# Kernel optimization log

Hardware: AMD Instinct MI355X
Metric: run time of the kernel (lower is better)

Reference implementation:

```python
import jax, jax.numpy as jnp
import numpy as np

GRID = 24          # grid_size = sqrt(N-1)
N = GRID * GRID + 1
C = 768
H = 12
D = C // H
WINDOW = 7
B = 32


def build_local_mask(seq_len, grid_size, window_size):
    # patch (row, col) coordinates for tokens 1..N-1
    idx = np.arange(seq_len - 1)
    row = idx // grid_size
    col = idx % grid_size
    r = window_size // 2
    # local window: |dr| <= r and |dc| <= r (matches the torch double loop)
    patch_mask = (np.abs(row[:, None] - row[None, :]) <= r) & \
                 (np.abs(col[:, None] - col[None, :]) <= r)
    mask = np.zeros((seq_len, seq_len), dtype=bool)
    mask[1:, 1:] = patch_mask
    mask[0, :] = True   # CLS attends to all
    mask[:, 0] = True   # all attend to CLS
    return jnp.asarray(mask)


def setup_inputs() -> dict:
    key = jax.random.key(0)
    kx, kqkv, kproj = jax.random.split(key, 3)
    x = jax.random.normal(kx, (B, N, C), dtype=jnp.float32)
    W_qkv = jax.random.normal(kqkv, (C, 3 * C), dtype=jnp.float32) * 0.02
    W_proj = jax.random.normal(kproj, (C, C), dtype=jnp.float32) * 0.02
    b_proj = jnp.zeros((C,), dtype=jnp.float32)
    mask = build_local_mask(N, GRID, WINDOW)
    return {"x": x, "W_qkv": W_qkv, "W_proj": W_proj, "b_proj": b_proj, "mask": mask}


def reference(x, W_qkv, W_proj, b_proj, mask):
    Bb, Nn, Cc = x.shape
    scale = 1.0 / jnp.sqrt(jnp.asarray(D, dtype=x.dtype))
    qkv = (x @ W_qkv).reshape(Bb, Nn, 3, H, D)
    qkv = jnp.transpose(qkv, (2, 0, 3, 1, 4))  # [3, B, H, N, D]
    q, k, v = qkv[0], qkv[1], qkv[2]
    attn = jnp.einsum('bhnd,bhmd->bhnm', q, k) * scale
    attn = jnp.where(mask[None, None, :, :], attn, jnp.asarray(-jnp.inf, dtype=attn.dtype))
    attn = jax.nn.softmax(attn, axis=-1)
    out = jnp.einsum('bhnm,bhmd->bhnd', attn, v)  # [B, H, N, D]
    out = jnp.transpose(out, (0, 2, 1, 3)).reshape(Bb, Nn, Cc)
    return out @ W_proj + b_proj
```

## Files before the change

kernel.cpp:

```cpp
#include <hip/hip_runtime.h>
#include <stdint.h>

#define GRID_S 24
#define NTOK   577
#define CDIM   768
#define HEADS  12
#define DHEAD  64
#define BATCH  32

#define MREAL  (BATCH*NTOK)
#define MTILES 145
#define MPAD   (MTILES*128)
#define KDIM   768
#define NQKV   2304
#define VTP    584

typedef __attribute__((ext_vector_type(4))) float         f32x4;
typedef __attribute__((ext_vector_type(8))) short         s16x8;
typedef __attribute__((ext_vector_type(4))) unsigned int  u32x4;
typedef __attribute__((address_space(1))) const void g_void;
typedef __attribute__((address_space(3))) void lds_void;

__device__ __forceinline__ unsigned short f2bf(float f) {
    unsigned int u = __float_as_uint(f);
    u += 0x7fffu + ((u >> 16) & 1u);
    return (unsigned short)(u >> 16);
}
__device__ __forceinline__ float bf2f(unsigned short h) {
    return __uint_as_float(((unsigned int)h) << 16);
}

extern "C" __global__ void __launch_bounds__(256)
k_cast_x(const float* __restrict__ x, unsigned short* __restrict__ xb) {
    const long long n4 = (long long)MPAD * CDIM / 4;
    const long long v4 = (long long)MREAL * CDIM / 4;
    long long i = (long long)blockIdx.x * blockDim.x + threadIdx.x;
    const long long stride = (long long)gridDim.x * blockDim.x;
    for (; i < n4; i += stride) {
        float4 v = (i < v4) ? ((const float4*)x)[i] : make_float4(0.f, 0.f, 0.f, 0.f);
        ushort4 o;
        o.x = f2bf(v.x); o.y = f2bf(v.y); o.z = f2bf(v.z); o.w = f2bf(v.w);
        ((ushort4*)xb)[i] = o;
    }
}

extern "C" __global__ void __launch_bounds__(256)
k_tcast(const float* __restrict__ W, unsigned short* __restrict__ WT, int ncol, int n) {
    int i = blockIdx.x * blockDim.x + threadIdx.x;
    const int stride = gridDim.x * blockDim.x;
    for (; i < n; i += stride) {
        const int c = i / KDIM;
        const int k = i - c * KDIM;
        WT[i] = f2bf(W[(long long)k * ncol + c]);
    }
}

__device__ __forceinline__ void gemm_core(const unsigned short* __restrict__ A,
                                          const unsigned short* __restrict__ BT,
                                          int m0, int n0,
                                          unsigned short* As, unsigned short* Bs,
                                          f32x4 acc[4][4]) {
    const int tid  = threadIdx.x;
    const int lane = tid & 63;
    const int wid  = tid >> 6;
    const int wm = wid >> 1, wn = wid & 1;
    const int lrow = lane & 15;
    const int kh   = (lane >> 4) * 8;
    const int srow = (lane >> 2);
    const int scol = (lane & 3) * 16;

#pragma unroll
    for (int i = 0; i < 4; i++)
#pragma unroll
        for (int j = 0; j < 4; j++)
            acc[i][j] = (f32x4){0.f, 0.f, 0.f, 0.f};

    for (int k0 = 0; k0 < KDIM; k0 += 32) {
#pragma unroll
        for (int c = 0; c < 2; ++c) {
            const int chunk = wid * 2 + c;
            const int row   = chunk * 16 + srow;
            const char* ga = (const char*)(A  + (long long)(m0 + row) * KDIM + k0) + scol;
            const char* gb = (const char*)(BT + (long long)(n0 + row) * KDIM + k0) + scol;
            __builtin_amdgcn_global_load_lds((g_void*)ga, (lds_void*)((char*)As + chunk * 1024), 16, 0, 0);
            __builtin_amdgcn_global_load_lds((g_void*)gb, (lds_void*)((char*)Bs + chunk * 1024), 16, 0, 0);
        }
        __syncthreads();

        s16x8 af[4], bq[4];
#pragma unroll
        for (int f = 0; f < 4; ++f) {
            af[f] = *(const s16x8*)(As + (wm * 64 + f * 16 + lrow) * 32 + kh);
            bq[f] = *(const s16x8*)(Bs + (wn * 64 + f * 16 + lrow) * 32 + kh);
        }
#pragma unroll
        for (int i = 0; i < 4; i++)
#pragma unroll
            for (int j = 0; j < 4; j++)
                acc[i][j] = __builtin_amdgcn_mfma_f32_16x16x32_bf16(af[i], bq[j], acc[i][j], 0, 0, 0);
        __syncthreads();
    }
}

extern "C" __global__ void __launch_bounds__(256)
k_gemm_qkv(const unsigned short* __restrict__ A, const unsigned short* __restrict__ BT,
           unsigned short* __restrict__ Qb, unsigned short* __restrict__ Kb,
           unsigned short* __restrict__ Vb) {
    __shared__ unsigned short As[128 * 32];
    __shared__ unsigned short Bs[128 * 32];
    const int m0 = blockIdx.x * 128;
    const int n0 = blockIdx.y * 128;
    f32x4 acc[4][4];
    gemm_core(A, BT, m0, n0, As, Bs, acc);

    const int lane = threadIdx.x & 63;
    const int wid  = threadIdx.x >> 6;
    const int wm = wid >> 1, wn = wid & 1;
    const int lrow = lane & 15;
#pragma unroll
    for (int fi = 0; fi < 4; ++fi) {
        const int mbase = m0 + wm * 64 + fi * 16 + (lane >> 4) * 4;
#pragma unroll
        for (int fj = 0; fj < 4; ++fj) {
            const int cb  = n0 + wn * 64 + fj * 16;
            const int s   = cb / 768;
            const int rem = cb - s * 768;
            const int h   = rem >> 6;
            const int d   = (rem & 63) + lrow;
            const float sc = (s == 0) ? 0.125f : 1.0f;
            unsigned short* dst = (s == 0) ? Qb : (s == 1) ? Kb : Vb;
#pragma unroll
            for (int i = 0; i < 4; i++) {
                const int m = mbase + i;
                if (m < MREAL) {
                    const int b  = m / NTOK;
                    const int nn = m - b * NTOK;
                    dst[(((long long)(b * HEADS + h)) * NTOK + nn) * DHEAD + d] = f2bf(acc[fi][fj][i] * sc);
                }
            }
        }
    }
}

extern "C" __global__ void __launch_bounds__(256)
k_gemm_proj(const unsigned short* __restrict__ A, const unsigned short* __restrict__ BT,
            const float* __restrict__ bias, float* __restrict__ out) {
    __shared__ unsigned short As[128 * 32];
    __shared__ unsigned short Bs[128 * 32];
    const int m0 = blockIdx.x * 128;
    const int n0 = blockIdx.y * 128;
    f32x4 acc[4][4];
    gemm_core(A, BT, m0, n0, As, Bs, acc);

    const int lane = threadIdx.x & 63;
    const int wid  = threadIdx.x >> 6;
    const int wm = wid >> 1, wn = wid & 1;
    const int lrow = lane & 15;
#pragma unroll
    for (int fi = 0; fi < 4; ++fi) {
        const int mbase = m0 + wm * 64 + fi * 16 + (lane >> 4) * 4;
#pragma unroll
        for (int fj = 0; fj < 4; ++fj) {
            const int col = n0 + wn * 64 + fj * 16 + lrow;
            const float bv = bias[col];
#pragma unroll
            for (int i = 0; i < 4; i++) {
                const int m = mbase + i;
                if (m < MREAL) out[(long long)m * CDIM + col] = acc[fi][fj][i] + bv;
            }
        }
    }
}

extern "C" __global__ void __launch_bounds__(256)
k_vtrans(const unsigned short* __restrict__ Vb, unsigned short* __restrict__ Vt) {
    const int NB = 145;
    const int total = 384 * 64 * NB;
    int idx = blockIdx.x * 256 + threadIdx.x;
    if (idx >= total) return;
    const int bh = idx / (64 * NB);
    const int r  = idx - bh * 64 * NB;
    const int d  = r / NB;
    const int nb = r - d * NB;
    const int n0 = nb * 4 + 1;
    const unsigned short* src = Vb + ((long long)bh * NTOK) * 64 + d;
    ushort4 o;
    o.x = src[(long long)min(n0 + 0, NTOK - 1) * 64];
    o.y = src[(long long)min(n0 + 1, NTOK - 1) * 64];
    o.z = src[(long long)min(n0 + 2, NTOK - 1) * 64];
    o.w = src[(long long)min(n0 + 3, NTOK - 1) * 64];
    *(ushort4*)(Vt + ((long long)bh * 64 + d) * VTP + (n0 - 1)) = o;
}

extern "C" __global__ void __launch_bounds__(256)
k_attn2(const unsigned short* __restrict__ Qb, const unsigned short* __restrict__ Kb,
        const unsigned short* __restrict__ Vb, const unsigned short* __restrict__ Vt,
        unsigned short* __restrict__ AO) {
    const int l   = threadIdx.x & 63;
    const int w   = threadIdx.x >> 6;
    const int bh  = blockIdx.x;
    const int qt  = blockIdx.y;
    const int qbase = qt * 64 + w * 16;
    if (qbase >= NTOK) return;
    const int q15 = l & 15;
    const int hi  = l >> 4;
    const int kh  = hi * 8;

    const unsigned short* Qh  = Qb + (long long)bh * NTOK * 64;
    const unsigned short* Kh  = Kb + (long long)bh * NTOK * 64;
    const unsigned short* Vbh = Vb + (long long)bh * NTOK * 64;
    const unsigned short* Vh  = Vt + (long long)bh * 64 * VTP;

    const int qn_frag = min(qbase + q15, NTOK - 1);
    const s16x8 qf0 = *(const s16x8*)(Qh + (long long)qn_frag * 64 + kh);
    const s16x8 qf1 = *(const s16x8*)(Qh + (long long)qn_frag * 64 + 32 + kh);

    const int q_n = qbase + q15;
    const bool q_is_cls = (q_n == 0);
    int pr = 0, pc = 0;
    {
        const int p = (q_n >= 1 ? min(q_n, NTOK - 1) : 1) - 1;
        pr = p / GRID_S; pc = p - pr * GRID_S;
    }

    int ks, ke;
    if (qbase == 0) { ks = 1; ke = NTOK; }
    else {
        const int nlo = qbase, nhi = min(qbase + 15, NTOK - 1);
        const int prmin = (nlo - 1) / GRID_S, prmax = (nhi - 1) / GRID_S;
        const int rlo = max(0, prmin - 3), rhi = min(GRID_S - 1, prmax + 3);
        ks = 1 + rlo * GRID_S; ke = 1 + (rhi + 1) * GRID_S;
    }

    float s0 = 0.f;
    {
        const s16x8 k0a = *(const s16x8*)(Kh + kh);
        const s16x8 k0b = *(const s16x8*)(Kh + 32 + kh);
#pragma unroll
        for (int j = 0; j < 8; ++j) {
            s0 += bf2f((unsigned short)qf0[j]) * bf2f((unsigned short)k0a[j]);
            s0 += bf2f((unsigned short)qf1[j]) * bf2f((unsigned short)k0b[j]);
        }
    }
    s0 += __shfl_xor(s0, 16, 64);
    s0 += __shfl_xor(s0, 32, 64);
    const float e0 = __expf(s0);

    float e0q[4];
#pragma unroll
    for (int i = 0; i < 4; ++i) e0q[i] = __shfl(e0, (hi << 2) + i, 64);

    f32x4 Oacc[4];
#pragma unroll
    for (int dt = 0; dt < 4; ++dt) {
        const float v0 = bf2f(Vbh[dt * 16 + q15]);
        f32x4 t; t[0] = e0q[0]*v0; t[1] = e0q[1]*v0; t[2] = e0q[2]*v0; t[3] = e0q[3]*v0;
        Oacc[dt] = t;
    }

    float dsum = 0.f;
    const int nch = (ke - ks + 31) >> 5;
    for (int ch = 0; ch < nch; ++ch) {
        const int cb = ks + (ch << 5);
        f32x4 ct0 = (f32x4){0,0,0,0}, ct1 = (f32x4){0,0,0,0};

#define QK_TILE(TB, CT) {                                                          \
            const int key = min((TB) + q15, NTOK - 1);                             \
            const unsigned short* kp_ = Kh + (long long)key * 64 + kh;             \
            const s16x8 ka  = *(const s16x8*)kp_;                                  \
            const s16x8 kb2 = *(const s16x8*)(kp_ + 32);                           \
            f32x4 c = __builtin_amdgcn_mfma_f32_16x16x32_bf16(ka,  qf0, (f32x4){0,0,0,0}, 0,0,0); \
            c = __builtin_amdgcn_mfma_f32_16x16x32_bf16(kb2, qf1, c, 0,0,0);       \
            _Pragma("unroll")                                                      \
            for (int i = 0; i < 4; ++i) {                                          \
                const int kk  = (TB) + (hi << 2) + i;                              \
                const int kpp = kk - 1;                                            \
                const int kr  = kpp / GRID_S;                                      \
                const int kc  = kpp - kr * GRID_S;                                 \
                const bool win = ((unsigned)(kr - pr + 3) <= 6u) && ((unsigned)(kc - pc + 3) <= 6u); \
                const bool valid = (kk < ke) && (q_is_cls || win);                 \
                const float e = valid ? __expf(c[i]) : 0.f;                        \
                CT[i] = e; dsum += e;                                              \
            } }

        QK_TILE(cb, ct0)
        if (cb + 16 < ke) QK_TILE(cb + 16, ct1)
#undef QK_TILE

        float pv[8];
#pragma unroll
        for (int j = 0; j < 8; ++j) {
            const int src = ((((hi & 1) << 3) + j) >> 2) * 16 + q15;
            const float a0 = __shfl(ct0[j & 3], src, 64);
            const float a1 = __shfl(ct1[j & 3], src, 64);
            pv[j] = (hi & 2) ? a1 : a0;
        }
        u32x4 paw;
#pragma unroll
        for (int t = 0; t < 4; ++t)
            paw[t] = (unsigned)f2bf(pv[2 * t]) | ((unsigned)f2bf(pv[2 * t + 1]) << 16);
        const s16x8 pa16 = __builtin_bit_cast(s16x8, paw);

        const int gvb = cb - 1 + kh;
#pragma unroll
        for (int dt = 0; dt < 4; ++dt) {
            const s16x8 vf = *(const s16x8*)(Vh + (long long)(dt * 16 + q15) * VTP + gvb);
            Oacc[dt] = __builtin_amdgcn_mfma_f32_16x16x32_bf16(pa16, vf, Oacc[dt], 0, 0, 0);
        }
    }

    dsum += __shfl_xor(dsum, 16, 64);
    dsum += __shfl_xor(dsum, 32, 64);
    const float tot = e0 + dsum;
    float rq[4];
#pragma unroll
    for (int i = 0; i < 4; ++i) rq[i] = 1.f / __shfl(tot, (hi << 2) + i, 64);

    const int b = bh / HEADS, h = bh - b * HEADS;
#pragma unroll
    for (int i = 0; i < 4; ++i) {
        const int n = qbase + (hi << 2) + i;
        if (n < NTOK) {
#pragma unroll
            for (int dt = 0; dt < 4; ++dt)
                AO[((long long)(b * NTOK + n)) * CDIM + h * 64 + dt * 16 + q15] =
                    f2bf(Oacc[dt][i] * rq[i]);
        }
    }
}

extern "C" void kernel_launch(void* const* d_in, const int* in_sizes, int n_in,
                              void* d_out, int out_size, void* d_ws, size_t ws_size,
                              hipStream_t stream) {
    (void)in_sizes; (void)n_in; (void)out_size; (void)ws_size;
    const float* x     = (const float*)d_in[0];
    const float* Wqkv  = (const float*)d_in[1];
    const float* Wproj = (const float*)d_in[2];
    const float* bproj = (const float*)d_in[3];
    float* out = (float*)d_out;
    char*  ws  = (char*)d_ws;

    unsigned short* xb  = (unsigned short*)(ws);
    unsigned short* wqT = (unsigned short*)(ws + 28508160LL);
    unsigned short* wpT = (unsigned short*)(ws + 32047104LL);
    unsigned short* Qb  = (unsigned short*)(ws + 33226752LL);
    unsigned short* Kb  = (unsigned short*)(ws + 61593600LL);
    unsigned short* Vb  = (unsigned short*)(ws + 89960448LL);
    unsigned short* AO  = (unsigned short*)(ws + 118327296LL);
    unsigned short* Vt  = (unsigned short*)(ws);

    hipLaunchKernelGGL(k_cast_x,  dim3(2048), dim3(256), 0, stream, x, xb);
    hipLaunchKernelGGL(k_tcast,   dim3(2048), dim3(256), 0, stream, Wqkv, wqT, NQKV, KDIM * NQKV);
    hipLaunchKernelGGL(k_tcast,   dim3(1024), dim3(256), 0, stream, Wproj, wpT, CDIM, KDIM * CDIM);
    hipLaunchKernelGGL(k_gemm_qkv, dim3(MTILES, NQKV / 128), dim3(256), 0, stream, xb, wqT, Qb, Kb, Vb);
    hipLaunchKernelGGL(k_vtrans,  dim3((384 * 64 * 145 + 255) / 256), dim3(256), 0, stream, Vb, Vt);
    hipLaunchKernelGGL(k_attn2,   dim3(384, 10), dim3(256), 0, stream, Qb, Kb, Vb, Vt, AO);
    hipLaunchKernelGGL(k_gemm_proj, dim3(MTILES, CDIM / 128), dim3(256), 0, stream, AO, wpT, bproj, out);
}
```

Before: 417.6 us.

## Double-buffer GEMM LDS tiles and transpose V through an LDS tile

```diff
diff --git a/kernel.cpp b/kernel.cpp
--- a/kernel.cpp
+++ b/kernel.cpp
@@ -75,23 +75,30 @@
         for (int j = 0; j < 4; j++)
             acc[i][j] = (f32x4){0.f, 0.f, 0.f, 0.f};
 
-    for (int k0 = 0; k0 < KDIM; k0 += 32) {
-#pragma unroll
-        for (int c = 0; c < 2; ++c) {
-            const int chunk = wid * 2 + c;
-            const int row   = chunk * 16 + srow;
-            const char* ga = (const char*)(A  + (long long)(m0 + row) * KDIM + k0) + scol;
-            const char* gb = (const char*)(BT + (long long)(n0 + row) * KDIM + k0) + scol;
-            __builtin_amdgcn_global_load_lds((g_void*)ga, (lds_void*)((char*)As + chunk * 1024), 16, 0, 0);
-            __builtin_amdgcn_global_load_lds((g_void*)gb, (lds_void*)((char*)Bs + chunk * 1024), 16, 0, 0);
-        }
-        __syncthreads();
-
+#define STAGE(buf, k0) { _Pragma("unroll")                                             \
+    for (int c = 0; c < 2; ++c) {                                                      \
+        const int chunk = wid * 2 + c;                               \
+        const int row   = chunk * 16 + srow;                                           \
+        const char* ga = (const char*)(A  + (long long)(m0 + row) * KDIM + (k0)) + scol; \
+        const char* gb = (const char*)(BT + (long long)(n0 + row) * KDIM + (k0)) + scol; \
+        __builtin_amdgcn_global_load_lds((g_void*)ga, (lds_void*)((char*)As + (buf) * 8192 + chunk * 1024), 16, 0, 0); \
+        __builtin_amdgcn_global_load_lds((g_void*)gb, (lds_void*)((char*)Bs + (buf) * 8192 + chunk * 1024), 16, 0, 0); \
+    } }
+
+    STAGE(0, 0)
+    __syncthreads();
+
+    for (int step = 0; step < KDIM / 32; ++step) {
+        const int buf = step & 1;
+        if (step + 1 < KDIM / 32) STAGE(buf ^ 1, (step + 1) * 32)
+
+        const unsigned short* Ab = As + buf * 4096;
+        const unsigned short* Bb = Bs + buf * 4096;
         s16x8 af[4], bq[4];
 #pragma unroll
         for (int f = 0; f < 4; ++f) {
-            af[f] = *(const s16x8*)(As + (wm * 64 + f * 16 + lrow) * 32 + kh);
-            bq[f] = *(const s16x8*)(Bs + (wn * 64 + f * 16 + lrow) * 32 + kh);
+            af[f] = *(const s16x8*)(Ab + (wm * 64 + f * 16 + lrow) * 32 + kh);
+            bq[f] = *(const s16x8*)(Bb + (wn * 64 + f * 16 + lrow) * 32 + kh);
         }
 #pragma unroll
         for (int i = 0; i < 4; i++)
@@ -100,14 +107,15 @@
                 acc[i][j] = __builtin_amdgcn_mfma_f32_16x16x32_bf16(af[i], bq[j], acc[i][j], 0, 0, 0);
         __syncthreads();
     }
+#undef STAGE
 }
 
 extern "C" __global__ void __launch_bounds__(256)
 k_gemm_qkv(const unsigned short* __restrict__ A, const unsigned short* __restrict__ BT,
            unsigned short* __restrict__ Qb, unsigned short* __restrict__ Kb,
            unsigned short* __restrict__ Vb) {
-    __shared__ unsigned short As[128 * 32];
-    __shared__ unsigned short Bs[128 * 32];
+    __shared__ unsigned short As[2 * 128 * 32];
+    __shared__ unsigned short Bs[2 * 128 * 32];
     const int m0 = blockIdx.x * 128;
     const int n0 = blockIdx.y * 128;
     f32x4 acc[4][4];
@@ -145,8 +153,8 @@
 extern "C" __global__ void __launch_bounds__(256)
 k_gemm_proj(const unsigned short* __restrict__ A, const unsigned short* __restrict__ BT,
             const float* __restrict__ bias, float* __restrict__ out) {
-    __shared__ unsigned short As[128 * 32];
-    __shared__ unsigned short Bs[128 * 32];
+    __shared__ unsigned short As[2 * 128 * 32];
+    __shared__ unsigned short Bs[2 * 128 * 32];
     const int m0 = blockIdx.x * 128;
     const int n0 = blockIdx.y * 128;
     f32x4 acc[4][4];
@@ -174,22 +182,33 @@
 
 extern "C" __global__ void __launch_bounds__(256)
 k_vtrans(const unsigned short* __restrict__ Vb, unsigned short* __restrict__ Vt) {
-    const int NB = 145;
-    const int total = 384 * 64 * NB;
-    int idx = blockIdx.x * 256 + threadIdx.x;
-    if (idx >= total) return;
-    const int bh = idx / (64 * NB);
-    const int r  = idx - bh * 64 * NB;
-    const int d  = r / NB;
-    const int nb = r - d * NB;
-    const int n0 = nb * 4 + 1;
-    const unsigned short* src = Vb + ((long long)bh * NTOK) * 64 + d;
-    ushort4 o;
-    o.x = src[(long long)min(n0 + 0, NTOK - 1) * 64];
-    o.y = src[(long long)min(n0 + 1, NTOK - 1) * 64];
-    o.z = src[(long long)min(n0 + 2, NTOK - 1) * 64];
-    o.w = src[(long long)min(n0 + 3, NTOK - 1) * 64];
-    *(ushort4*)(Vt + ((long long)bh * 64 + d) * VTP + (n0 - 1)) = o;
+    __shared__ unsigned short S[64 * 66];
+    const int bh = blockIdx.x;
+    const int n0 = 1 + blockIdx.y * 64;
+    const int t  = threadIdx.x;
+    {
+        const int tr = t >> 2, cq = t & 3;
+        const unsigned short* src = Vb + ((long long)bh * NTOK + n0 + tr) * 64 + cq * 16;
+        ushort4 a0 = *(const ushort4*)(src + 0);
+        ushort4 a1 = *(const ushort4*)(src + 4);
+        ushort4 a2 = *(const ushort4*)(src + 8);
+        ushort4 a3 = *(const ushort4*)(src + 12);
+        unsigned short* dl = S + tr * 66 + cq * 16;
+        dl[0]=a0.x; dl[1]=a0.y; dl[2]=a0.z; dl[3]=a0.w;
+        dl[4]=a1.x; dl[5]=a1.y; dl[6]=a1.z; dl[7]=a1.w;
+        dl[8]=a2.x; dl[9]=a2.y; dl[10]=a2.z; dl[11]=a2.w;
+        dl[12]=a3.x; dl[13]=a3.y; dl[14]=a3.z; dl[15]=a3.w;
+    }
+    __syncthreads();
+    {
+        const int dr = t >> 2, tq = t & 3;
+        unsigned short o[16];
+#pragma unroll
+        for (int j = 0; j < 16; ++j) o[j] = S[(tq * 16 + j) * 66 + dr];
+        unsigned short* dst = Vt + ((long long)bh * 64 + dr) * VTP + (n0 - 1) + tq * 16;
+#pragma unroll
+        for (int j = 0; j < 16; ++j) dst[j] = o[j];
+    }
 }
 
 extern "C" __global__ void __launch_bounds__(256)
@@ -353,7 +372,7 @@
     hipLaunchKernelGGL(k_tcast,   dim3(2048), dim3(256), 0, stream, Wqkv, wqT, NQKV, KDIM * NQKV);
     hipLaunchKernelGGL(k_tcast,   dim3(1024), dim3(256), 0, stream, Wproj, wpT, CDIM, KDIM * CDIM);
     hipLaunchKernelGGL(k_gemm_qkv, dim3(MTILES, NQKV / 128), dim3(256), 0, stream, xb, wqT, Qb, Kb, Vb);
-    hipLaunchKernelGGL(k_vtrans,  dim3((384 * 64 * 145 + 255) / 256), dim3(256), 0, stream, Vb, Vt);
+    hipLaunchKernelGGL(k_vtrans,  dim3(384, 9), dim3(256), 0, stream, Vb, Vt);
     hipLaunchKernelGGL(k_attn2,   dim3(384, 10), dim3(256), 0, stream, Qb, Kb, Vb, Vt, AO);
     hipLaunchKernelGGL(k_gemm_proj, dim3(MTILES, CDIM / 128), dim3(256), 0, stream, AO, wpT, bproj, out);
 }
```

Result: faster. 382.0 us (-8.5%).
